# Kernel tuning notes

Measured on AMD Instinct MI355X. Metric: run time of the kernel, lower is better.

The kernel has to match this reference:

```python
import jax, jax.numpy as jnp
import numpy as np

B, LQ, LA, D, H = 8, 2048, 2048, 300, 150

def setup_inputs() -> dict:
    key = jax.random.key(0)
    ks = jax.random.split(key, 6)
    return {
        "Q": jax.random.normal(ks[0], (B, LQ, D), dtype=jnp.float32),
        "A": jax.random.normal(ks[1], (B, LA, D), dtype=jnp.float32),
        "Wi": jax.random.normal(ks[2], (D, H), dtype=jnp.float32) * (1.0 / np.sqrt(D)),
        "Wu": jax.random.normal(ks[3], (D, H), dtype=jnp.float32) * (1.0 / np.sqrt(D)),
        "Wg": jax.random.normal(ks[4], (H, H), dtype=jnp.float32) * (1.0 / np.sqrt(H)),
        "Wt": jax.random.normal(ks[5], (2 * H, H), dtype=jnp.float32) * (1.0 / np.sqrt(2 * H)),
        "bi": jnp.zeros((H,), dtype=jnp.float32),
        "bu": jnp.zeros((H,), dtype=jnp.float32),
        "bg": jnp.zeros((H,), dtype=jnp.float32),
        "bt": jnp.zeros((H,), dtype=jnp.float32),
    }

def reference(Q, A, Wi, Wu, Wg, Wt, bi, bu, bg, bt):
    # sigmoid/tanh gated projections (shared weights for Q and A)
    def gate(X):
        return jax.nn.sigmoid(X @ Wi + bi) * jnp.tanh(X @ Wu + bu)
    Qh = gate(Q)  # [B, LQ, H]
    Ah = gate(A)  # [B, LA, H]
    # attention scores G[b,q,a] = <(Qh Wg + bg)[b,q], Ah[b,a]>
    G = jnp.einsum('bqh,bah->bqa', Qh @ Wg + bg, Ah)
    G = jax.nn.softmax(G, axis=1)  # softmax over Q positions
    # H[b,a] = sum_q G[b,q,a] * Qh[b,q]
    Hm = jnp.einsum('bqa,bqh->bah', G, Qh)  # [B, LA, H]
    # 'nn' comparison: relu(concat([Ah, Hm]) @ Wt + bt)
    T = jax.nn.relu(jnp.concatenate([Ah, Hm], axis=-1) @ Wt + bt)
    return T
```

## Files before the change

### kernel.cpp

```cpp
#include <hip/hip_runtime.h>
#include <math.h>

#define BB 8
#define LQ 2048
#define DD 300
#define HHH 150
#define NROWS (BB * LQ)

#define KP 168
#define QTS 72
#define WCE 27136
#define SLAB_B 45056
#define SLAB_E 22528
#define QHT_OFF_E 11008

typedef __bf16 bf16x8 __attribute__((ext_vector_type(8)));
typedef __bf16 bf16x4 __attribute__((ext_vector_type(4)));
typedef float f32x16 __attribute__((ext_vector_type(16)));

__device__ __forceinline__ void gl_lds16(const void* g, void* l) {
    __builtin_amdgcn_global_load_lds(
        (const __attribute__((address_space(1))) void*)g,
        (__attribute__((address_space(3))) void*)l,
        16, 0, 0);
}
__device__ __forceinline__ void stage_flat(const void* g, void* l, int bytes,
                                           int w, int lane) {
    for (int ofs = w * 1024; ofs < bytes; ofs += 4096)
        gl_lds16((const char*)g + ofs + lane * 16, (char*)l + ofs);
}
__device__ __forceinline__ f32x16 z16() {
    f32x16 v;
#pragma unroll
    for (int i = 0; i < 16; i++) v[i] = 0.f;
    return v;
}
__device__ __forceinline__ bf16x8 cvt8(float4 u, float4 v) {
    return (bf16x8){(__bf16)u.x, (__bf16)u.y, (__bf16)u.z, (__bf16)u.w,
                    (__bf16)v.x, (__bf16)v.y, (__bf16)v.z, (__bf16)v.w};
}

__global__ __launch_bounds__(256) void convert_weights(
    const float* __restrict__ Wi, const float* __restrict__ Wu,
    const float* __restrict__ Wg, const float* __restrict__ Wt,
    __bf16* __restrict__ WiC, __bf16* __restrict__ WuC,
    __bf16* __restrict__ WgT, __bf16* __restrict__ Wt12)
{
    const int z = blockIdx.y;
    const int i = blockIdx.x * 256 + threadIdx.x;
    if (z < 2) {
        if (i >= 2 * WCE) return;
        int c = i / WCE, rem = i - c * WCE;
        float v = 0.f;
        if (rem < 160 * KP) {
            int h = rem / KP, kc = rem - h * KP;
            int d = c * 160 + kc;
            if (kc < 160 && d < DD && h < HHH) v = (z ? Wu : Wi)[(size_t)d * HHH + h];
        }
        (z ? WuC : WiC)[i] = (__bf16)v;
    } else if (z == 2) {
        if (i >= WCE) return;
        float v = 0.f;
        if (i < 160 * KP) {
            int h = i / KP, kc = i - h * KP;
            if (kc < HHH && h < HHH) v = Wg[(size_t)kc * HHH + h];
        }
        WgT[i] = (__bf16)v;
    } else {
        if (i >= 2 * 160 * KP) return;
        int c = i / (160 * KP), rem = i - c * (160 * KP);
        int h = rem / KP, kc = rem - h * KP;
        float v = (kc < HHH && h < HHH) ? Wt[(size_t)(c * HHH + kc) * HHH + h] : 0.f;
        Wt12[i] = (__bf16)v;
    }
}

__global__ __launch_bounds__(256, 1) void gatep(
    const float* __restrict__ Q, const float* __restrict__ A,
    const __bf16* __restrict__ WiC, const __bf16* __restrict__ WuC,
    const __bf16* __restrict__ WgT,
    const float* __restrict__ bi, const float* __restrict__ bu,
    const float* __restrict__ bg,
    __bf16* __restrict__ AhB, __bf16* __restrict__ Slab)
{
    __shared__ __align__(16) __bf16 WB[2][WCE];
    __shared__ __align__(16) __bf16 QhA[128 * KP];
    const int tid = threadIdx.x;
    const int w = tid >> 6, lane = tid & 63;
    const int m32 = lane & 31, half = lane >> 5;
    const int z = blockIdx.y;
    const int r0 = blockIdx.x * 128;
    const float* X = z ? A : Q;

    stage_flat(WiC, WB[0], 54272, w, lane);

    const float* xrow = X + (size_t)(r0 + w * 32 + m32) * DD + half * 8;
    bf16x8 af0[10], af1[10];
#pragma unroll
    for (int ks = 0; ks < 10; ks++) {
        float4 u = *(const float4*)(xrow + ks * 16);
        float4 v = *(const float4*)(xrow + ks * 16 + 4);
        af0[ks] = cvt8(u, v);
    }

    f32x16 ai[5], au[5];
#pragma unroll
    for (int t = 0; t < 5; t++) { ai[t] = z16(); au[t] = z16(); }

    __syncthreads();
    stage_flat(WuC, WB[1], 54272, w, lane);

#pragma unroll
    for (int ks = 0; ks < 8; ks++) {
        float4 u = *(const float4*)(xrow + 160 + ks * 16);
        float4 v = *(const float4*)(xrow + 160 + ks * 16 + 4);
        af1[ks] = cvt8(u, v);
    }
    {
        float4 u = *(const float4*)(xrow + 288);
        float4 v = (half == 0) ? *(const float4*)(xrow + 292) : (float4){0.f, 0.f, 0.f, 0.f};
        af1[8] = cvt8(u, v);
        af1[9] = (bf16x8){(__bf16)0.f, (__bf16)0.f, (__bf16)0.f, (__bf16)0.f,
                          (__bf16)0.f, (__bf16)0.f, (__bf16)0.f, (__bf16)0.f};
    }

    for (int ks = 0; ks < 10; ks++)
#pragma unroll
        for (int t = 0; t < 5; t++)
            ai[t] = __builtin_amdgcn_mfma_f32_32x32x16_bf16(
                af0[ks], *(const bf16x8*)(WB[0] + (t * 32 + m32) * KP + ks * 16 + half * 8),
                ai[t], 0, 0, 0);
    __syncthreads();
    stage_flat(WiC + WCE, WB[0], 54272, w, lane);
    for (int ks = 0; ks < 10; ks++)
#pragma unroll
        for (int t = 0; t < 5; t++)
            au[t] = __builtin_amdgcn_mfma_f32_32x32x16_bf16(
                af0[ks], *(const bf16x8*)(WB[1] + (t * 32 + m32) * KP + ks * 16 + half * 8),
                au[t], 0, 0, 0);
    __syncthreads();
    stage_flat(WuC + WCE, WB[1], 54272, w, lane);
    for (int ks = 0; ks < 10; ks++)
#pragma unroll
        for (int t = 0; t < 5; t++)
            ai[t] = __builtin_amdgcn_mfma_f32_32x32x16_bf16(
                af1[ks], *(const bf16x8*)(WB[0] + (t * 32 + m32) * KP + ks * 16 + half * 8),
                ai[t], 0, 0, 0);
    __syncthreads();
    if (z == 0) stage_flat(WgT, WB[0], 54272, w, lane);
    for (int ks = 0; ks < 10; ks++)
#pragma unroll
        for (int t = 0; t < 5; t++)
            au[t] = __builtin_amdgcn_mfma_f32_32x32x16_bf16(
                af1[ks], *(const bf16x8*)(WB[1] + (t * 32 + m32) * KP + ks * 16 + half * 8),
                au[t], 0, 0, 0);

#pragma unroll
    for (int t = 0; t < 5; t++) {
        int h = t * 32 + m32;
        int hc = h < HHH ? h : 0;
        float bih = bi[hc], buh = bu[hc];
#pragma unroll
        for (int r = 0; r < 16; r++) {
            float v = 0.f;
            if (h < HHH) {
                float xi = ai[t][r] + bih, xu = au[t][r] + buh;
                float s = 1.f / (1.f + __expf(-xi));
                float tt = 1.f - 2.f / (1.f + __expf(2.f * xu));
                v = s * tt;
            }
            ai[t][r] = v;
        }
    }

    if (z) {
#pragma unroll
        for (int t = 0; t < 5; t++) {
            int h = t * 32 + m32;
#pragma unroll
            for (int r = 0; r < 16; r++) {
                int rowp = (r & 3) + 8 * (r >> 2) + 4 * half;
                AhB[(size_t)(r0 + w * 32 + rowp) * KP + h] = (__bf16)ai[t][r];
            }
        }
        return;
    }

#pragma unroll
    for (int t = 0; t < 5; t++) {
        int h = t * 32 + m32;
#pragma unroll
        for (int r = 0; r < 16; r++) {
            int rowp = (r & 3) + 8 * (r >> 2) + 4 * half;
            QhA[(w * 32 + rowp) * KP + h] = (__bf16)ai[t][r];
        }
    }
    bf16x8 afq[10];
#pragma unroll
    for (int ks = 0; ks < 10; ks++)
        afq[ks] = *(const bf16x8*)(QhA + (w * 32 + m32) * KP + ks * 16 + half * 8);
    __syncthreads();

    f32x16 qg[5];
#pragma unroll
    for (int t = 0; t < 5; t++) qg[t] = z16();
    for (int ks = 0; ks < 10; ks++)
#pragma unroll
        for (int t = 0; t < 5; t++)
            qg[t] = __builtin_amdgcn_mfma_f32_32x32x16_bf16(
                afq[ks], *(const bf16x8*)(WB[0] + (t * 32 + m32) * KP + ks * 16 + half * 8),
                qg[t], 0, 0, 0);

    const int b = r0 >> 11, qt0 = (r0 & 2047) >> 6;
#pragma unroll
    for (int t = 0; t < 5; t++) {
        int h = t * 32 + m32;
        int hc = h < HHH ? h : 0;
        float bgh = bg[hc];
#pragma unroll
        for (int r = 0; r < 16; r++) {
            int rowp = (r & 3) + 8 * (r >> 2) + 4 * half;
            int q = (r0 & 2047) + w * 32 + rowp;
            float v = (h < HHH) ? (qg[t][r] + bgh) : 0.f;
            Slab[(size_t)(b * 32 + (q >> 6)) * SLAB_E + (q & 63) * KP + h] = (__bf16)v;
        }
    }

    {
        const int jl = tid & 63, tile = (tid >> 6) & 1, hgrp = tid >> 7;
        for (int hseg = hgrp; hseg < 20; hseg += 2) {
            bf16x8 vv = *(const bf16x8*)(QhA + (tile * 64 + jl) * KP + hseg * 8);
            __bf16* dst = Slab + (size_t)(b * 32 + qt0 + tile) * SLAB_E + QHT_OFF_E + jl;
#pragma unroll
            for (int e = 0; e < 8; e++)
                dst[(hseg * 8 + e) * QTS] = vv[e];
        }
    }
}

__global__ __launch_bounds__(256, 1) void attn_mfma(
    const __bf16* __restrict__ Slab, const __bf16* __restrict__ AhB,
    __bf16* __restrict__ O, float* __restrict__ L)
{
    __shared__ __align__(16) __bf16 AhS[128 * KP];
    __shared__ __align__(16) __bf16 Buf[2][SLAB_E];
    __shared__ __align__(16) __bf16 PS[128 * QTS];
    const int tid = threadIdx.x;
    const int w = tid >> 6, lane = tid & 63;
    const int m32 = lane & 31, half = lane >> 5;
    const int b = blockIdx.y, qh = blockIdx.z;
    const int a0 = blockIdx.x * 128;

    stage_flat(AhB + (size_t)(b * LQ + a0) * KP, AhS, 43008, w, lane);
    const char* slabBase = (const char*)Slab + (size_t)(b * 32 + qh * 16) * SLAB_B;
    stage_flat(slabBase, Buf[0], SLAB_B, w, lane);
    __syncthreads();

    bf16x8 af[10];
#pragma unroll
    for (int ks = 0; ks < 10; ks++)
        af[ks] = *(const bf16x8*)(AhS + (w * 32 + m32) * KP + ks * 16 + half * 8);

    float lsum[16];
#pragma unroll
    for (int r = 0; r < 16; r++) lsum[r] = 0.f;
    f32x16 acc[5];
#pragma unroll
    for (int t = 0; t < 5; t++) acc[t] = z16();

    for (int qt = 0; qt < 16; qt++) {
        const int cur = qt & 1;
        if (qt < 15)
            stage_flat(slabBase + (size_t)(qt + 1) * SLAB_B, Buf[cur ^ 1], SLAB_B, w, lane);
        const __bf16* Bq = Buf[cur];
        const __bf16* Bv = Buf[cur] + QHT_OFF_E;

        f32x16 s0 = z16(), s1 = z16();
        for (int ks = 0; ks < 10; ks++) {
            s0 = __builtin_amdgcn_mfma_f32_32x32x16_bf16(
                af[ks], *(const bf16x8*)(Bq + m32 * KP + ks * 16 + half * 8), s0, 0, 0, 0);
            s1 = __builtin_amdgcn_mfma_f32_32x32x16_bf16(
                af[ks], *(const bf16x8*)(Bq + (32 + m32) * KP + ks * 16 + half * 8), s1, 0, 0, 0);
        }
#pragma unroll
        for (int r = 0; r < 16; r++) {
            int rowp = (r & 3) + 8 * (r >> 2) + 4 * half;
            float p0 = __expf(s0[r]);
            float p1 = __expf(s1[r]);
            lsum[r] += p0 + p1;
            PS[(w * 32 + rowp) * QTS + m32] = (__bf16)p0;
            PS[(w * 32 + rowp) * QTS + 32 + m32] = (__bf16)p1;
        }
#pragma unroll
        for (int kk = 0; kk < 4; kk++) {
            bf16x8 pf = *(const bf16x8*)(PS + (w * 32 + m32) * QTS + kk * 16 + half * 8);
#pragma unroll
            for (int t = 0; t < 5; t++)
                acc[t] = __builtin_amdgcn_mfma_f32_32x32x16_bf16(
                    pf, *(const bf16x8*)(Bv + (t * 32 + m32) * QTS + kk * 16 + half * 8),
                    acc[t], 0, 0, 0);
        }
        __syncthreads();
    }

#pragma unroll
    for (int r = 0; r < 16; r++) {
        float s = lsum[r];
#pragma unroll
        for (int m = 1; m < 32; m <<= 1) s += __shfl_xor(s, m, 64);
        lsum[r] = s;
    }
    __bf16* Ob = O + (size_t)(qh * NROWS + b * LQ + a0) * 160;
#pragma unroll
    for (int t = 0; t < 5; t++) {
        int h = t * 32 + m32;
#pragma unroll
        for (int r = 0; r < 16; r++) {
            int rowp = (r & 3) + 8 * (r >> 2) + 4 * half;
            Ob[(size_t)(w * 32 + rowp) * 160 + h] = (__bf16)acc[t][r];
        }
    }
    if (m32 == 0) {
        float* Lb = L + qh * NROWS + b * LQ + a0 + w * 32;
#pragma unroll
        for (int r = 0; r < 16; r++) {
            int rowp = (r & 3) + 8 * (r >> 2) + 4 * half;
            Lb[rowp] = lsum[r];
        }
    }
}

__global__ __launch_bounds__(256, 1) void final_mfma(
    const __bf16* __restrict__ AhB, const __bf16* __restrict__ O,
    const float* __restrict__ L, const __bf16* __restrict__ Wt12,
    const float* __restrict__ bt, float* __restrict__ Out)
{
    __shared__ __align__(16) __bf16 AS[64 * KP];
    __shared__ __align__(16) __bf16 HS[64 * KP];
    __shared__ __align__(16) __bf16 WtS[2 * 160 * KP];
    const int tid = threadIdx.x;
    const int w = tid >> 6, lane = tid & 63;
    const int m32 = lane & 31, half = lane >> 5;
    const int r0 = blockIdx.x * 64;

    stage_flat(AhB + (size_t)r0 * KP, AS, 21504, w, lane);
    stage_flat(Wt12, WtS, 107520, w, lane);

    {
        int rhat = tid >> 2, qq = tid & 3;
        int grow = r0 + rhat;
        float inv = 1.f / (L[grow] + L[NROWS + grow]);
        const bf16x8* o1 = (const bf16x8*)(O + (size_t)grow * 160 + qq * 40);
        const bf16x8* o2 = (const bf16x8*)(O + (size_t)(NROWS + grow) * 160 + qq * 40);
#pragma unroll
        for (int k = 0; k < 5; k++) {
            bf16x8 x = o1[k], y = o2[k], hv;
#pragma unroll
            for (int j = 0; j < 8; j++)
                hv[j] = (__bf16)(((float)x[j] + (float)y[j]) * inv);
            *(bf16x8*)(HS + rhat * KP + qq * 40 + k * 8) = hv;
        }
    }
    __syncthreads();

    const int m = w & 1, th = w >> 1;
    const int tbase = th ? 3 : 0, tn = th ? 2 : 3;
    f32x16 acc[3];
#pragma unroll
    for (int i = 0; i < 3; i++) acc[i] = z16();

    for (int ch = 0; ch < 2; ch++) {
        const __bf16* src = ch ? HS : AS;
        for (int ks = 0; ks < 10; ks++) {
            bf16x8 af = *(const bf16x8*)(src + (m * 32 + m32) * KP + ks * 16 + half * 8);
#pragma unroll
            for (int ti = 0; ti < 3; ti++) {
                if (ti < tn) {
                    int t = tbase + ti;
                    acc[ti] = __builtin_amdgcn_mfma_f32_32x32x16_bf16(
                        af, *(const bf16x8*)(WtS + (ch * 160 + t * 32 + m32) * KP + ks * 16 + half * 8),
                        acc[ti], 0, 0, 0);
                }
            }
        }
    }

#pragma unroll
    for (int ti = 0; ti < 3; ti++) {
        if (ti < tn) {
            int t = tbase + ti;
            int h = t * 32 + m32;
            if (h < HHH) {
                float bth = bt[h];
#pragma unroll
                for (int r = 0; r < 16; r++) {
                    int rowp = (r & 3) + 8 * (r >> 2) + 4 * half;
                    float v = acc[ti][r] + bth;
                    Out[(size_t)(r0 + m * 32 + rowp) * HHH + h] = v > 0.f ? v : 0.f;
                }
            }
        }
    }
}

extern "C" void kernel_launch(void* const* d_in, const int* in_sizes, int n_in,
                              void* d_out, int out_size, void* d_ws, size_t ws_size,
                              hipStream_t stream)
{
    const float* Q  = (const float*)d_in[0];
    const float* A  = (const float*)d_in[1];
    const float* Wi = (const float*)d_in[2];
    const float* Wu = (const float*)d_in[3];
    const float* Wg = (const float*)d_in[4];
    const float* Wt = (const float*)d_in[5];
    const float* bi = (const float*)d_in[6];
    const float* bu = (const float*)d_in[7];
    const float* bg = (const float*)d_in[8];
    const float* bt = (const float*)d_in[9];
    float* out = (float*)d_out;

    char* ws = (char*)d_ws;
    __bf16* Slab = (__bf16*)(ws);
    __bf16* AhB  = (__bf16*)(ws + 11534336);
    __bf16* Op   = (__bf16*)(ws + 17039360);
    float*  Lp   = (float*) (ws + 27525120);
    __bf16* WiC  = (__bf16*)(ws + 27656192);
    __bf16* WuC  = (__bf16*)(ws + 27764736);
    __bf16* WgT  = (__bf16*)(ws + 27873280);
    __bf16* Wt12 = (__bf16*)(ws + 27927552);

    convert_weights<<<dim3(212, 4), 256, 0, stream>>>(Wi, Wu, Wg, Wt,
                                                      WiC, WuC, WgT, Wt12);
    gatep<<<dim3(NROWS / 128, 2), 256, 0, stream>>>(Q, A, WiC, WuC, WgT,
                                                    bi, bu, bg, AhB, Slab);
    attn_mfma<<<dim3(16, BB, 2), 256, 0, stream>>>(Slab, AhB, Op, Lp);
    final_mfma<<<NROWS / 64, 256, 0, stream>>>(AhB, Op, Lp, Wt12, bt, out);
}
```

Measured before the change: 169.1 us.

## Double waves per block in gate and attention kernels with split work

Both gatep and attn_mfma now launch 512 threads (8 waves) instead of 256. In gatep each wave covers a 32-row slice and only 2-3 of the 5 output column tiles, so each wave keeps fewer accumulators. In attn_mfma the extra waves split each Q tile's 64 columns in half, and the two halves write separate partial outputs and row sums, which final_mfma now adds across four partitions. The aim is more waves in flight per CU to hide latency and use fewer registers per wave, at the cost of a larger workspace and extra partial-output traffic in the final reduction.

Result: no change. 167.3 us (-1.1%).

```diff
diff --git a/kernel.cpp b/kernel.cpp
--- a/kernel.cpp
+++ b/kernel.cpp
@@ -27,6 +27,11 @@
 __device__ __forceinline__ void stage_flat(const void* g, void* l, int bytes,
                                            int w, int lane) {
     for (int ofs = w * 1024; ofs < bytes; ofs += 4096)
+        gl_lds16((const char*)g + ofs + lane * 16, (char*)l + ofs);
+}
+__device__ __forceinline__ void stage_flat8(const void* g, void* l, int bytes,
+                                            int w, int lane) {
+    for (int ofs = w * 1024; ofs < bytes; ofs += 8192)
         gl_lds16((const char*)g + ofs + lane * 16, (char*)l + ofs);
 }
 __device__ __forceinline__ f32x16 z16() {
@@ -75,7 +80,7 @@
     }
 }
 
-__global__ __launch_bounds__(256, 1) void gatep(
+__global__ __launch_bounds__(512, 2) void gatep(
     const float* __restrict__ Q, const float* __restrict__ A,
     const __bf16* __restrict__ WiC, const __bf16* __restrict__ WuC,
     const __bf16* __restrict__ WgT,
@@ -88,13 +93,15 @@
     const int tid = threadIdx.x;
     const int w = tid >> 6, lane = tid & 63;
     const int m32 = lane & 31, half = lane >> 5;
+    const int wm = w & 3, wn = w >> 2;
+    const int tof = wn ? 3 : 0, tn = wn ? 2 : 3;
     const int z = blockIdx.y;
     const int r0 = blockIdx.x * 128;
     const float* X = z ? A : Q;
 
-    stage_flat(WiC, WB[0], 54272, w, lane);
-
-    const float* xrow = X + (size_t)(r0 + w * 32 + m32) * DD + half * 8;
+    stage_flat8(WiC, WB[0], 54272, w, lane);
+
+    const float* xrow = X + (size_t)(r0 + wm * 32 + m32) * DD + half * 8;
     bf16x8 af0[10], af1[10];
 #pragma unroll
     for (int ks = 0; ks < 10; ks++) {
@@ -103,12 +110,12 @@
         af0[ks] = cvt8(u, v);
     }
 
-    f32x16 ai[5], au[5];
-#pragma unroll
-    for (int t = 0; t < 5; t++) { ai[t] = z16(); au[t] = z16(); }
-
-    __syncthreads();
-    stage_flat(WuC, WB[1], 54272, w, lane);
+    f32x16 ai[3], au[3];
+#pragma unroll
+    for (int t = 0; t < 3; t++) { ai[t] = z16(); au[t] = z16(); }
+
+    __syncthreads();
+    stage_flat8(WuC, WB[1], 54272, w, lane);
 
 #pragma unroll
     for (int ks = 0; ks < 8; ks++) {
@@ -126,109 +133,119 @@
 
     for (int ks = 0; ks < 10; ks++)
 #pragma unroll
-        for (int t = 0; t < 5; t++)
-            ai[t] = __builtin_amdgcn_mfma_f32_32x32x16_bf16(
-                af0[ks], *(const bf16x8*)(WB[0] + (t * 32 + m32) * KP + ks * 16 + half * 8),
-                ai[t], 0, 0, 0);
-    __syncthreads();
-    stage_flat(WiC + WCE, WB[0], 54272, w, lane);
-    for (int ks = 0; ks < 10; ks++)
-#pragma unroll
-        for (int t = 0; t < 5; t++)
-            au[t] = __builtin_amdgcn_mfma_f32_32x32x16_bf16(
-                af0[ks], *(const bf16x8*)(WB[1] + (t * 32 + m32) * KP + ks * 16 + half * 8),
-                au[t], 0, 0, 0);
-    __syncthreads();
-    stage_flat(WuC + WCE, WB[1], 54272, w, lane);
-    for (int ks = 0; ks < 10; ks++)
-#pragma unroll
-        for (int t = 0; t < 5; t++)
-            ai[t] = __builtin_amdgcn_mfma_f32_32x32x16_bf16(
-                af1[ks], *(const bf16x8*)(WB[0] + (t * 32 + m32) * KP + ks * 16 + half * 8),
-                ai[t], 0, 0, 0);
-    __syncthreads();
-    if (z == 0) stage_flat(WgT, WB[0], 54272, w, lane);
-    for (int ks = 0; ks < 10; ks++)
-#pragma unroll
-        for (int t = 0; t < 5; t++)
-            au[t] = __builtin_amdgcn_mfma_f32_32x32x16_bf16(
-                af1[ks], *(const bf16x8*)(WB[1] + (t * 32 + m32) * KP + ks * 16 + half * 8),
-                au[t], 0, 0, 0);
-
-#pragma unroll
-    for (int t = 0; t < 5; t++) {
-        int h = t * 32 + m32;
+        for (int ti = 0; ti < 3; ti++)
+            if (ti < tn)
+                ai[ti] = __builtin_amdgcn_mfma_f32_32x32x16_bf16(
+                    af0[ks], *(const bf16x8*)(WB[0] + ((tof + ti) * 32 + m32) * KP + ks * 16 + half * 8),
+                    ai[ti], 0, 0, 0);
+    __syncthreads();
+    stage_flat8(WiC + WCE, WB[0], 54272, w, lane);
+    for (int ks = 0; ks < 10; ks++)
+#pragma unroll
+        for (int ti = 0; ti < 3; ti++)
+            if (ti < tn)
+                au[ti] = __builtin_amdgcn_mfma_f32_32x32x16_bf16(
+                    af0[ks], *(const bf16x8*)(WB[1] + ((tof + ti) * 32 + m32) * KP + ks * 16 + half * 8),
+                    au[ti], 0, 0, 0);
+    __syncthreads();
+    stage_flat8(WuC + WCE, WB[1], 54272, w, lane);
+    for (int ks = 0; ks < 10; ks++)
+#pragma unroll
+        for (int ti = 0; ti < 3; ti++)
+            if (ti < tn)
+                ai[ti] = __builtin_amdgcn_mfma_f32_32x32x16_bf16(
+                    af1[ks], *(const bf16x8*)(WB[0] + ((tof + ti) * 32 + m32) * KP + ks * 16 + half * 8),
+                    ai[ti], 0, 0, 0);
+    __syncthreads();
+    if (z == 0) stage_flat8(WgT, WB[0], 54272, w, lane);
+    for (int ks = 0; ks < 10; ks++)
+#pragma unroll
+        for (int ti = 0; ti < 3; ti++)
+            if (ti < tn)
+                au[ti] = __builtin_amdgcn_mfma_f32_32x32x16_bf16(
+                    af1[ks], *(const bf16x8*)(WB[1] + ((tof + ti) * 32 + m32) * KP + ks * 16 + half * 8),
+                    au[ti], 0, 0, 0);
+
+#pragma unroll
+    for (int ti = 0; ti < 3; ti++) {
+        if (ti >= tn) continue;
+        int h = (tof + ti) * 32 + m32;
         int hc = h < HHH ? h : 0;
         float bih = bi[hc], buh = bu[hc];
 #pragma unroll
         for (int r = 0; r < 16; r++) {
             float v = 0.f;
             if (h < HHH) {
-                float xi = ai[t][r] + bih, xu = au[t][r] + buh;
+                float xi = ai[ti][r] + bih, xu = au[ti][r] + buh;
                 float s = 1.f / (1.f + __expf(-xi));
                 float tt = 1.f - 2.f / (1.f + __expf(2.f * xu));
                 v = s * tt;
             }
-            ai[t][r] = v;
+            ai[ti][r] = v;
         }
     }
 
     if (z) {
 #pragma unroll
-        for (int t = 0; t < 5; t++) {
-            int h = t * 32 + m32;
+        for (int ti = 0; ti < 3; ti++) {
+            if (ti >= tn) continue;
+            int h = (tof + ti) * 32 + m32;
 #pragma unroll
             for (int r = 0; r < 16; r++) {
                 int rowp = (r & 3) + 8 * (r >> 2) + 4 * half;
-                AhB[(size_t)(r0 + w * 32 + rowp) * KP + h] = (__bf16)ai[t][r];
+                AhB[(size_t)(r0 + wm * 32 + rowp) * KP + h] = (__bf16)ai[ti][r];
             }
         }
         return;
     }
 
 #pragma unroll
-    for (int t = 0; t < 5; t++) {
-        int h = t * 32 + m32;
+    for (int ti = 0; ti < 3; ti++) {
+        if (ti >= tn) continue;
+        int h = (tof + ti) * 32 + m32;
 #pragma unroll
         for (int r = 0; r < 16; r++) {
             int rowp = (r & 3) + 8 * (r >> 2) + 4 * half;
-            QhA[(w * 32 + rowp) * KP + h] = (__bf16)ai[t][r];
-        }
-    }
+            QhA[(wm * 32 + rowp) * KP + h] = (__bf16)ai[ti][r];
+        }
+    }
+    __syncthreads();
+
     bf16x8 afq[10];
 #pragma unroll
     for (int ks = 0; ks < 10; ks++)
-        afq[ks] = *(const bf16x8*)(QhA + (w * 32 + m32) * KP + ks * 16 + half * 8);
-    __syncthreads();
-
-    f32x16 qg[5];
-#pragma unroll
-    for (int t = 0; t < 5; t++) qg[t] = z16();
-    for (int ks = 0; ks < 10; ks++)
-#pragma unroll
-        for (int t = 0; t < 5; t++)
-            qg[t] = __builtin_amdgcn_mfma_f32_32x32x16_bf16(
-                afq[ks], *(const bf16x8*)(WB[0] + (t * 32 + m32) * KP + ks * 16 + half * 8),
-                qg[t], 0, 0, 0);
+        afq[ks] = *(const bf16x8*)(QhA + (wm * 32 + m32) * KP + ks * 16 + half * 8);
+
+    f32x16 qg[3];
+#pragma unroll
+    for (int t = 0; t < 3; t++) qg[t] = z16();
+    for (int ks = 0; ks < 10; ks++)
+#pragma unroll
+        for (int ti = 0; ti < 3; ti++)
+            if (ti < tn)
+                qg[ti] = __builtin_amdgcn_mfma_f32_32x32x16_bf16(
+                    afq[ks], *(const bf16x8*)(WB[0] + ((tof + ti) * 32 + m32) * KP + ks * 16 + half * 8),
+                    qg[ti], 0, 0, 0);
 
     const int b = r0 >> 11, qt0 = (r0 & 2047) >> 6;
 #pragma unroll
-    for (int t = 0; t < 5; t++) {
-        int h = t * 32 + m32;
+    for (int ti = 0; ti < 3; ti++) {
+        if (ti >= tn) continue;
+        int h = (tof + ti) * 32 + m32;
         int hc = h < HHH ? h : 0;
         float bgh = bg[hc];
 #pragma unroll
         for (int r = 0; r < 16; r++) {
             int rowp = (r & 3) + 8 * (r >> 2) + 4 * half;
-            int q = (r0 & 2047) + w * 32 + rowp;
-            float v = (h < HHH) ? (qg[t][r] + bgh) : 0.f;
+            int q = (r0 & 2047) + wm * 32 + rowp;
+            float v = (h < HHH) ? (qg[ti][r] + bgh) : 0.f;
             Slab[(size_t)(b * 32 + (q >> 6)) * SLAB_E + (q & 63) * KP + h] = (__bf16)v;
         }
     }
 
     {
         const int jl = tid & 63, tile = (tid >> 6) & 1, hgrp = tid >> 7;
-        for (int hseg = hgrp; hseg < 20; hseg += 2) {
+        for (int hseg = hgrp; hseg < 20; hseg += 4) {
             bf16x8 vv = *(const bf16x8*)(QhA + (tile * 64 + jl) * KP + hseg * 8);
             __bf16* dst = Slab + (size_t)(b * 32 + qt0 + tile) * SLAB_E + QHT_OFF_E + jl;
 #pragma unroll
@@ -238,28 +255,27 @@
     }
 }
 
-__global__ __launch_bounds__(256, 1) void attn_mfma(
+__global__ __launch_bounds__(512, 2) void attn_mfma(
     const __bf16* __restrict__ Slab, const __bf16* __restrict__ AhB,
     __bf16* __restrict__ O, float* __restrict__ L)
 {
-    __shared__ __align__(16) __bf16 AhS[128 * KP];
     __shared__ __align__(16) __bf16 Buf[2][SLAB_E];
     __shared__ __align__(16) __bf16 PS[128 * QTS];
     const int tid = threadIdx.x;
     const int w = tid >> 6, lane = tid & 63;
     const int m32 = lane & 31, half = lane >> 5;
+    const int wa = w & 3, wx = w >> 2;
     const int b = blockIdx.y, qh = blockIdx.z;
     const int a0 = blockIdx.x * 128;
 
-    stage_flat(AhB + (size_t)(b * LQ + a0) * KP, AhS, 43008, w, lane);
     const char* slabBase = (const char*)Slab + (size_t)(b * 32 + qh * 16) * SLAB_B;
-    stage_flat(slabBase, Buf[0], SLAB_B, w, lane);
-    __syncthreads();
-
+    stage_flat8(slabBase, Buf[0], SLAB_B, w, lane);
+
+    const __bf16* arow = AhB + (size_t)(b * LQ + a0 + wa * 32 + m32) * KP + half * 8;
     bf16x8 af[10];
 #pragma unroll
     for (int ks = 0; ks < 10; ks++)
-        af[ks] = *(const bf16x8*)(AhS + (w * 32 + m32) * KP + ks * 16 + half * 8);
+        af[ks] = *(const bf16x8*)(arow + ks * 16);
 
     float lsum[16];
 #pragma unroll
@@ -267,37 +283,36 @@
     f32x16 acc[5];
 #pragma unroll
     for (int t = 0; t < 5; t++) acc[t] = z16();
+    __syncthreads();
 
     for (int qt = 0; qt < 16; qt++) {
         const int cur = qt & 1;
         if (qt < 15)
-            stage_flat(slabBase + (size_t)(qt + 1) * SLAB_B, Buf[cur ^ 1], SLAB_B, w, lane);
+            stage_flat8(slabBase + (size_t)(qt + 1) * SLAB_B, Buf[cur ^ 1], SLAB_B, w, lane);
         const __bf16* Bq = Buf[cur];
         const __bf16* Bv = Buf[cur] + QHT_OFF_E;
 
-        f32x16 s0 = z16(), s1 = z16();
-        for (int ks = 0; ks < 10; ks++) {
-            s0 = __builtin_amdgcn_mfma_f32_32x32x16_bf16(
-                af[ks], *(const bf16x8*)(Bq + m32 * KP + ks * 16 + half * 8), s0, 0, 0, 0);
-            s1 = __builtin_amdgcn_mfma_f32_32x32x16_bf16(
-                af[ks], *(const bf16x8*)(Bq + (32 + m32) * KP + ks * 16 + half * 8), s1, 0, 0, 0);
-        }
+        f32x16 s = z16();
+        for (int ks = 0; ks < 10; ks++)
+            s = __builtin_amdgcn_mfma_f32_32x32x16_bf16(
+                af[ks], *(const bf16x8*)(Bq + (wx * 32 + m32) * KP + ks * 16 + half * 8),
+                s, 0, 0, 0);
+
 #pragma unroll
         for (int r = 0; r < 16; r++) {
             int rowp = (r & 3) + 8 * (r >> 2) + 4 * half;
-            float p0 = __expf(s0[r]);
-            float p1 = __expf(s1[r]);
-            lsum[r] += p0 + p1;
-            PS[(w * 32 + rowp) * QTS + m32] = (__bf16)p0;
-            PS[(w * 32 + rowp) * QTS + 32 + m32] = (__bf16)p1;
-        }
-#pragma unroll
-        for (int kk = 0; kk < 4; kk++) {
-            bf16x8 pf = *(const bf16x8*)(PS + (w * 32 + m32) * QTS + kk * 16 + half * 8);
+            float p = __expf(s[r]);
+            lsum[r] += p;
+            PS[(wa * 32 + rowp) * QTS + wx * 32 + m32] = (__bf16)p;
+        }
+
+#pragma unroll
+        for (int kkL = 0; kkL < 2; kkL++) {
+            bf16x8 pf = *(const bf16x8*)(PS + (wa * 32 + m32) * QTS + (wx * 2 + kkL) * 16 + half * 8);
 #pragma unroll
             for (int t = 0; t < 5; t++)
                 acc[t] = __builtin_amdgcn_mfma_f32_32x32x16_bf16(
-                    pf, *(const bf16x8*)(Bv + (t * 32 + m32) * QTS + kk * 16 + half * 8),
+                    pf, *(const bf16x8*)(Bv + (t * 32 + m32) * QTS + (wx * 2 + kkL) * 16 + half * 8),
                     acc[t], 0, 0, 0);
         }
         __syncthreads();
@@ -310,18 +325,19 @@
         for (int m = 1; m < 32; m <<= 1) s += __shfl_xor(s, m, 64);
         lsum[r] = s;
     }
-    __bf16* Ob = O + (size_t)(qh * NROWS + b * LQ + a0) * 160;
+    const int part = qh * 2 + wx;
+    __bf16* Ob = O + ((size_t)part * NROWS + b * LQ + a0 + wa * 32) * 160;
 #pragma unroll
     for (int t = 0; t < 5; t++) {
         int h = t * 32 + m32;
 #pragma unroll
         for (int r = 0; r < 16; r++) {
             int rowp = (r & 3) + 8 * (r >> 2) + 4 * half;
-            Ob[(size_t)(w * 32 + rowp) * 160 + h] = (__bf16)acc[t][r];
+            Ob[(size_t)rowp * 160 + h] = (__bf16)acc[t][r];
         }
     }
     if (m32 == 0) {
-        float* Lb = L + qh * NROWS + b * LQ + a0 + w * 32;
+        float* Lb = L + (size_t)part * NROWS + b * LQ + a0 + wa * 32;
 #pragma unroll
         for (int r = 0; r < 16; r++) {
             int rowp = (r & 3) + 8 * (r >> 2) + 4 * half;
@@ -349,15 +365,21 @@
     {
         int rhat = tid >> 2, qq = tid & 3;
         int grow = r0 + rhat;
-        float inv = 1.f / (L[grow] + L[NROWS + grow]);
-        const bf16x8* o1 = (const bf16x8*)(O + (size_t)grow * 160 + qq * 40);
-        const bf16x8* o2 = (const bf16x8*)(O + (size_t)(NROWS + grow) * 160 + qq * 40);
+        float inv = 1.f / (L[grow] + L[NROWS + grow] + L[2 * NROWS + grow] + L[3 * NROWS + grow]);
 #pragma unroll
         for (int k = 0; k < 5; k++) {
-            bf16x8 x = o1[k], y = o2[k], hv;
-#pragma unroll
-            for (int j = 0; j < 8; j++)
-                hv[j] = (__bf16)(((float)x[j] + (float)y[j]) * inv);
+            float sum[8];
+#pragma unroll
+            for (int j = 0; j < 8; j++) sum[j] = 0.f;
+#pragma unroll
+            for (int p = 0; p < 4; p++) {
+                bf16x8 x = *(const bf16x8*)(O + ((size_t)p * NROWS + grow) * 160 + qq * 40 + k * 8);
+#pragma unroll
+                for (int j = 0; j < 8; j++) sum[j] += (float)x[j];
+            }
+            bf16x8 hv;
+#pragma unroll
+            for (int j = 0; j < 8; j++) hv[j] = (__bf16)(sum[j] * inv);
             *(bf16x8*)(HS + rhat * KP + qq * 40 + k * 8) = hv;
         }
     }
@@ -423,16 +445,16 @@
     __bf16* Slab = (__bf16*)(ws);
     __bf16* AhB  = (__bf16*)(ws + 11534336);
     __bf16* Op   = (__bf16*)(ws + 17039360);
-    float*  Lp   = (float*) (ws + 27525120);
-    __bf16* WiC  = (__bf16*)(ws + 27656192);
-    __bf16* WuC  = (__bf16*)(ws + 27764736);
-    __bf16* WgT  = (__bf16*)(ws + 27873280);
-    __bf16* Wt12 = (__bf16*)(ws + 27927552);
+    float*  Lp   = (float*) (ws + 38010880);
+    __bf16* WiC  = (__bf16*)(ws + 38273024);
+    __bf16* WuC  = (__bf16*)(ws + 38381568);
+    __bf16* WgT  = (__bf16*)(ws + 38490112);
+    __bf16* Wt12 = (__bf16*)(ws + 38544384);
 
     convert_weights<<<dim3(212, 4), 256, 0, stream>>>(Wi, Wu, Wg, Wt,
                                                       WiC, WuC, WgT, Wt12);
-    gatep<<<dim3(NROWS / 128, 2), 256, 0, stream>>>(Q, A, WiC, WuC, WgT,
+    gatep<<<dim3(NROWS / 128, 2), 512, 0, stream>>>(Q, A, WiC, WuC, WgT,
                                                     bi, bu, bg, AhB, Slab);
-    attn_mfma<<<dim3(16, BB, 2), 256, 0, stream>>>(Slab, AhB, Op, Lp);
+    attn_mfma<<<dim3(16, BB, 2), 512, 0, stream>>>(Slab, AhB, Op, Lp);
     final_mfma<<<NROWS / 64, 256, 0, stream>>>(AhB, Op, Lp, Wt12, bt, out);
 }
```
